# Kernel optimization log

Measured on AMD Instinct MI355X. Metric: run time of the kernel, lower is better.

## Reference

```python
import jax, jax.numpy as jnp
import numpy as np

B, S, D = 4, 512, 256
H_SP, W_SP = 64, 64
NUM_HEADS = 8
HEAD_DIM = D // NUM_HEADS


def setup_inputs() -> dict:
    key = jax.random.key(0)
    ks = jax.random.split(key, 10)
    scale = 1.0 / np.sqrt(D)
    return {
        "query": jax.random.normal(ks[0], (B, S, D), dtype=jnp.float32),
        "key_value": jax.random.normal(ks[1], (B, D, H_SP, W_SP), dtype=jnp.float32),
        "Wq": jax.random.normal(ks[2], (D, D), dtype=jnp.float32) * scale,
        "bq": jnp.zeros((D,), dtype=jnp.float32),
        "Wk": jax.random.normal(ks[3], (D, D), dtype=jnp.float32) * scale,
        "bk": jnp.zeros((D,), dtype=jnp.float32),
        "Wv": jax.random.normal(ks[4], (D, D), dtype=jnp.float32) * scale,
        "bv": jnp.zeros((D,), dtype=jnp.float32),
        "Wo": jax.random.normal(ks[5], (D, D), dtype=jnp.float32) * scale,
        "bo": jnp.zeros((D,), dtype=jnp.float32),
    }


def reference(query, key_value, Wq, bq, Wk, bk, Wv, bv, Wo, bo):
    # query: (B, S, D); key_value: (B, D, H, W)
    b, d, h, w = key_value.shape
    s = query.shape[1]
    hw = h * w
    kv = key_value.reshape(b, d, hw).transpose(0, 2, 1)  # (B, HW, D)

    # Linear projections (torch Linear: x @ W.T + b)
    Q = query @ Wq.T + bq                                # (B, S, D)
    K = kv @ Wk.T + bk                                   # (B, HW, D)
    V = kv @ Wv.T + bv                                   # (B, HW, D)

    # Split heads: (B, nH, len, hd)
    Qh = Q.reshape(b, s, NUM_HEADS, HEAD_DIM).transpose(0, 2, 1, 3)
    Kh = K.reshape(b, hw, NUM_HEADS, HEAD_DIM).transpose(0, 2, 1, 3)
    Vh = V.reshape(b, hw, NUM_HEADS, HEAD_DIM).transpose(0, 2, 1, 3)

    scale = HEAD_DIM ** -0.5
    # NOTE: _add_spatial_attention is dead code (returns attn unchanged);
    # norm1/norm2 are never applied in forward; dropout is identity in eval.
    attn = jnp.einsum('bhsd,bhkd->bhsk', Qh, Kh) * scale  # (B, nH, S, HW)
    attn = jax.nn.softmax(attn, axis=-1)
    out = jnp.einsum('bhsk,bhkd->bhsd', attn, Vh)         # (B, nH, S, hd)
    out = out.transpose(0, 2, 1, 3).reshape(b, s, d)      # (B, S, D)
    return out @ Wo.T + bo
```

## Files before the change

### kernel.cpp

```cpp
#include <hip/hip_runtime.h>

constexpr int B_  = 4;
constexpr int S_  = 512;
constexpr int D_  = 256;
constexpr int HW_ = 4096;
constexpr int NH_ = 8;
constexpr int HD_ = 32;
constexpr int NSPLIT = 2;
constexpr int ROWS_  = B_ * NH_ * S_;
constexpr int KVB    = 64;
constexpr int TILES  = HW_ / NSPLIT / KVB;

typedef float  f32x4  __attribute__((ext_vector_type(4)));
typedef short  s16x4  __attribute__((ext_vector_type(4)));
typedef short  s16x8  __attribute__((ext_vector_type(8)));
typedef __bf16 bf16x8 __attribute__((ext_vector_type(8)));

__device__ __forceinline__ f32x4 mfma_bf16(s16x8 a, s16x8 b, f32x4 c) {
  return __builtin_amdgcn_mfma_f32_16x16x32_bf16(
      __builtin_bit_cast(bf16x8, a), __builtin_bit_cast(bf16x8, b), c, 0, 0, 0);
}

__device__ __forceinline__ void split4(float4 v, s16x4& h, s16x4& l) {
  float x[4] = {v.x, v.y, v.z, v.w};
  #pragma unroll
  for (int j = 0; j < 4; ++j) {
    unsigned xb = __float_as_uint(x[j]);
    h[j] = (short)(xb >> 16);
    float lo = x[j] - __uint_as_float(xb & 0xFFFF0000u);
    l[j] = (short)((__float_as_uint(lo) + 0x8000u) >> 16);
  }
}

__global__ __launch_bounds__(256)
void transpose_split(const float* __restrict__ KV,
                     short* __restrict__ Th, short* __restrict__ Tl)
{
  __shared__ float tile[64][65];
  const int bid = blockIdx.x;
  const int hwb = bid & 63;
  const int db  = (bid >> 6) & 3;
  const int b   = bid >> 8;
  const int hw0 = hwb * 64, d0 = db * 64;
  const int tid = threadIdx.x;
  #pragma unroll
  for (int i = 0; i < 4; ++i) {
    const int idx = tid + (i << 8);
    const int d = idx >> 4, h4 = idx & 15;
    *(float4*)&tile[d][h4 * 4] =
        *(const float4*)&KV[((size_t)(b * D_ + d0 + d)) * HW_ + hw0 + h4 * 4];
  }
  __syncthreads();
  #pragma unroll
  for (int i = 0; i < 4; ++i) {
    const int idx = tid + (i << 8);
    const int hw = idx >> 4, d4 = idx & 15;
    const float4 v = make_float4(tile[d4*4+0][hw], tile[d4*4+1][hw],
                                 tile[d4*4+2][hw], tile[d4*4+3][hw]);
    s16x4 hh, ll; split4(v, hh, ll);
    const size_t o = ((size_t)(b * HW_ + hw0 + hw)) * D_ + d0 + d4 * 4;
    *(s16x4*)&Th[o] = hh; *(s16x4*)&Tl[o] = ll;
  }
}

template<bool ASPLIT, bool DUAL, bool OSPLIT>
__global__ __launch_bounds__(256)
void gemm_mfma(const float* __restrict__ Af,
               const short* __restrict__ Ah_, const short* __restrict__ Al_,
               const float* __restrict__ W0, const float* __restrict__ b0,
               float* __restrict__ C0f, short* __restrict__ C0h, short* __restrict__ C0l,
               const float* __restrict__ W1, const float* __restrict__ b1,
               short* __restrict__ C1h, short* __restrict__ C1l,
               int M, float alpha)
{
  union Sm {
    struct {
      short Ah[64][40], Al[64][40];
      short W0h[64][40], W0l[64][40];
      short W1h[64][40], W1l[64][40];
    } s;
    float ep[64][76];
  };
  __shared__ __align__(16) Sm sm;

  const int tid = threadIdx.x;
  const int wv = tid >> 6, lane = tid & 63, lq = lane & 15, lg = lane >> 4;
  const int wm = wv >> 1, wn = wv & 1;
  const int nx = M >> 6;
  int bid = blockIdx.x;
  bid = (bid & 7) * ((nx << 2) >> 3) + (bid >> 3);
  const int xm = bid % nx, yn = bid / nx;
  const int m0 = xm << 6, n0 = yn << 6;

  f32x4 acc0[2][2] = {};
  f32x4 acc1[2][2] = {};

  s16x8 aH, aL;
  float4 aF[2], w0R[2], w1R[2];

  auto gload = [&](int kt) {
    const int k0 = kt << 5;
    if constexpr (ASPLIT) {
      const int m = tid >> 2, c8 = tid & 3;
      const size_t off = (size_t)(m0 + m) * D_ + k0 + c8 * 8;
      aH = *(const s16x8*)&Ah_[off];
      aL = *(const s16x8*)&Al_[off];
    } else {
      #pragma unroll
      for (int i = 0; i < 2; ++i) {
        const int idx = tid + (i << 8);
        const int m = idx >> 3, c4 = idx & 7;
        aF[i] = *(const float4*)&Af[(size_t)(m0 + m) * D_ + k0 + c4 * 4];
      }
    }
    #pragma unroll
    for (int i = 0; i < 2; ++i) {
      const int idx = tid + (i << 8);
      const int n = idx >> 3, c4 = idx & 7;
      w0R[i] = *(const float4*)&W0[(size_t)(n0 + n) * D_ + k0 + c4 * 4];
      if constexpr (DUAL)
        w1R[i] = *(const float4*)&W1[(size_t)(n0 + n) * D_ + k0 + c4 * 4];
    }
  };

  auto stage = [&]() {
    if constexpr (ASPLIT) {
      const int m = tid >> 2, c8 = tid & 3;
      *(s16x8*)&sm.s.Ah[m][c8 * 8] = aH;
      *(s16x8*)&sm.s.Al[m][c8 * 8] = aL;
    } else {
      #pragma unroll
      for (int i = 0; i < 2; ++i) {
        const int idx = tid + (i << 8);
        const int m = idx >> 3, c4 = idx & 7;
        s16x4 hh, ll; split4(aF[i], hh, ll);
        *(s16x4*)&sm.s.Ah[m][c4 * 4] = hh;
        *(s16x4*)&sm.s.Al[m][c4 * 4] = ll;
      }
    }
    #pragma unroll
    for (int i = 0; i < 2; ++i) {
      const int idx = tid + (i << 8);
      const int n = idx >> 3, c4 = idx & 7;
      float4 w = w0R[i];
      w.x *= alpha; w.y *= alpha; w.z *= alpha; w.w *= alpha;
      s16x4 hh, ll; split4(w, hh, ll);
      *(s16x4*)&sm.s.W0h[n][c4 * 4] = hh;
      *(s16x4*)&sm.s.W0l[n][c4 * 4] = ll;
      if constexpr (DUAL) {
        split4(w1R[i], hh, ll);
        *(s16x4*)&sm.s.W1h[n][c4 * 4] = hh;
        *(s16x4*)&sm.s.W1l[n][c4 * 4] = ll;
      }
    }
  };

  gload(0);
  #pragma unroll
  for (int kt = 0; kt < 8; ++kt) {
    __syncthreads();
    stage();
    __syncthreads();
    if (kt < 7) gload(kt + 1);
    s16x8 ah[2], al[2];
    #pragma unroll
    for (int mi = 0; mi < 2; ++mi) {
      ah[mi] = *(const s16x8*)&sm.s.Ah[wm * 32 + mi * 16 + lq][lg * 8];
      al[mi] = *(const s16x8*)&sm.s.Al[wm * 32 + mi * 16 + lq][lg * 8];
    }
    #pragma unroll
    for (int ni = 0; ni < 2; ++ni) {
      const int nr = wn * 32 + ni * 16 + lq;
      const s16x8 bh = *(const s16x8*)&sm.s.W0h[nr][lg * 8];
      const s16x8 bl = *(const s16x8*)&sm.s.W0l[nr][lg * 8];
      #pragma unroll
      for (int mi = 0; mi < 2; ++mi) {
        acc0[mi][ni] = mfma_bf16(ah[mi], bh, acc0[mi][ni]);
        acc0[mi][ni] = mfma_bf16(al[mi], bh, acc0[mi][ni]);
        acc0[mi][ni] = mfma_bf16(ah[mi], bl, acc0[mi][ni]);
      }
      if constexpr (DUAL) {
        const s16x8 ch = *(const s16x8*)&sm.s.W1h[nr][lg * 8];
        const s16x8 cl = *(const s16x8*)&sm.s.W1l[nr][lg * 8];
        #pragma unroll
        for (int mi = 0; mi < 2; ++mi) {
          acc1[mi][ni] = mfma_bf16(ah[mi], ch, acc1[mi][ni]);
          acc1[mi][ni] = mfma_bf16(al[mi], ch, acc1[mi][ni]);
          acc1[mi][ni] = mfma_bf16(ah[mi], cl, acc1[mi][ni]);
        }
      }
    }
  }

  __syncthreads();
  #pragma unroll
  for (int mi = 0; mi < 2; ++mi)
    #pragma unroll
    for (int ni = 0; ni < 2; ++ni)
      #pragma unroll
      for (int r = 0; r < 4; ++r)
        sm.ep[wm*32 + mi*16 + lg*4 + r][wn*32 + ni*16 + lq] = acc0[mi][ni][r];
  __syncthreads();
  #pragma unroll
  for (int i = 0; i < 4; ++i) {
    const int idx = tid + (i << 8);
    const int m = idx >> 4, c4 = idx & 15;
    const float4 v = *(const float4*)&sm.ep[m][c4 * 4];
    const float4 bb = *(const float4*)&b0[n0 + c4 * 4];
    const float4 o = make_float4(v.x + alpha * bb.x, v.y + alpha * bb.y,
                                 v.z + alpha * bb.z, v.w + alpha * bb.w);
    const size_t off = (size_t)(m0 + m) * D_ + n0 + c4 * 4;
    if constexpr (OSPLIT) {
      s16x4 hh, ll; split4(o, hh, ll);
      *(s16x4*)&C0h[off] = hh;
      *(s16x4*)&C0l[off] = ll;
    } else {
      *(float4*)&C0f[off] = o;
    }
  }

  if constexpr (DUAL) {
    __syncthreads();
    #pragma unroll
    for (int mi = 0; mi < 2; ++mi)
      #pragma unroll
      for (int ni = 0; ni < 2; ++ni)
        *(f32x4*)&sm.ep[wn*32 + ni*16 + lq][wm*32 + mi*16 + lg*4] = acc1[mi][ni];
    __syncthreads();
    const int b = m0 >> 12, hw0 = m0 & (HW_ - 1);
    #pragma unroll
    for (int i = 0; i < 4; ++i) {
      const int idx = tid + (i << 8);
      const int n = idx >> 4, m4 = idx & 15;
      const float4 v = *(const float4*)&sm.ep[n][m4 * 4];
      const float bb = b1[n0 + n];
      const float4 o = make_float4(v.x + bb, v.y + bb, v.z + bb, v.w + bb);
      s16x4 hh, ll; split4(o, hh, ll);
      const size_t off = ((size_t)(b * D_ + n0 + n)) * HW_ + hw0 + m4 * 4;
      *(s16x4*)&C1h[off] = hh;
      *(s16x4*)&C1l[off] = ll;
    }
  }
}

__global__ __launch_bounds__(256)
void attn_mfma(const short* __restrict__ Qh_, const short* __restrict__ Ql_,
               const short* __restrict__ Kh_, const short* __restrict__ Kl_,
               const short* __restrict__ Vth, const short* __restrict__ Vtl,
               float* __restrict__ Opart, float* __restrict__ Ml)
{
  union SmemT {
    struct {
      short Kh[KVB][40], Kl[KVB][40];
      short Vh[HD_][72], Vl[HD_][72];
      short Ph[4][16][72], Pl[4][16][72];
    } a;
    float ep[4][16][36];
  };
  __shared__ __align__(16) SmemT sm;

  const int tid  = threadIdx.x;
  const int wv   = tid >> 6, lane = tid & 63;
  const int lq   = lane & 15, lg = lane >> 4;

  int bid = blockIdx.x;
  bid = (bid & 7) * 64 + (bid >> 3);
  const int qt = bid & 7;
  const int h  = (bid >> 3) & 7;
  const int b  = (bid >> 6) & 3;
  const int sp = bid >> 8;
  const int q0 = qt * 64;

  s16x8 qh, ql;
  {
    const size_t qb = ((size_t)(b * S_ + q0 + wv * 16 + lq)) * D_ + h * HD_ + lg * 8;
    qh = *(const s16x8*)&Qh_[qb];
    ql = *(const s16x8*)&Ql_[qb];
  }

  float mrun = -1e30f, lrun = 0.f;
  f32x4 o0 = {0.f, 0.f, 0.f, 0.f}, o1 = {0.f, 0.f, 0.f, 0.f};

  s16x8 krH, krL, vrH, vrL;
  const int key = tid >> 2, c8k = tid & 3;
  const int dd  = tid >> 3, c8v = tid & 7;
  auto gload = [&](int t) {
    const size_t kb = ((size_t)(b * HW_ + t * KVB + key)) * D_ + h * HD_ + c8k * 8;
    krH = *(const s16x8*)&Kh_[kb];
    krL = *(const s16x8*)&Kl_[kb];
    const size_t vb = ((size_t)(b * D_ + h * HD_ + dd)) * HW_ + t * KVB + c8v * 8;
    vrH = *(const s16x8*)&Vth[vb];
    vrL = *(const s16x8*)&Vtl[vb];
  };

  gload(sp * TILES);
  for (int tt = 0; tt < TILES; ++tt) {
    __syncthreads();
    *(s16x8*)&sm.a.Kh[key][c8k * 8] = krH;
    *(s16x8*)&sm.a.Kl[key][c8k * 8] = krL;
    *(s16x8*)&sm.a.Vh[dd][c8v * 8]  = vrH;
    *(s16x8*)&sm.a.Vl[dd][c8v * 8]  = vrL;
    __syncthreads();
    if (tt + 1 < TILES) gload(sp * TILES + tt + 1);

    f32x4 sc4[4];
    #pragma unroll
    for (int c = 0; c < 4; ++c) {
      const s16x8 ah = *(const s16x8*)&sm.a.Kh[c * 16 + lq][lg * 8];
      const s16x8 al = *(const s16x8*)&sm.a.Kl[c * 16 + lq][lg * 8];
      f32x4 acc = {0.f, 0.f, 0.f, 0.f};
      acc = mfma_bf16(ah, qh, acc);
      acc = mfma_bf16(al, qh, acc);
      acc = mfma_bf16(ah, ql, acc);
      sc4[c] = acc;
    }

    float mt = sc4[0][0];
    #pragma unroll
    for (int c = 0; c < 4; ++c)
      #pragma unroll
      for (int r = 0; r < 4; ++r) mt = fmaxf(mt, sc4[c][r]);
    mt = fmaxf(mt, __shfl_xor(mt, 16));
    mt = fmaxf(mt, __shfl_xor(mt, 32));
    const float nm = fmaxf(mrun, mt);
    const float fr = __expf(mrun - nm);
    mrun = nm;
    o0 *= fr; o1 *= fr;
    float ps = 0.f;
    #pragma unroll
    for (int c = 0; c < 4; ++c) {
      float4 p;
      p.x = __expf(sc4[c][0] - nm);
      p.y = __expf(sc4[c][1] - nm);
      p.z = __expf(sc4[c][2] - nm);
      p.w = __expf(sc4[c][3] - nm);
      ps += p.x + p.y + p.z + p.w;
      s16x4 ph, pl;
      split4(p, ph, pl);
      *(s16x4*)&sm.a.Ph[wv][lq][c * 16 + lg * 4] = ph;
      *(s16x4*)&sm.a.Pl[wv][lq][c * 16 + lg * 4] = pl;
    }
    ps += __shfl_xor(ps, 16);
    ps += __shfl_xor(ps, 32);
    lrun = lrun * fr + ps;

    #pragma unroll
    for (int c2 = 0; c2 < 2; ++c2) {
      const s16x8 ph = *(const s16x8*)&sm.a.Ph[wv][lq][c2 * 32 + lg * 8];
      const s16x8 pl = *(const s16x8*)&sm.a.Pl[wv][lq][c2 * 32 + lg * 8];
      {
        const s16x8 vh = *(const s16x8*)&sm.a.Vh[lq][c2 * 32 + lg * 8];
        const s16x8 vl = *(const s16x8*)&sm.a.Vl[lq][c2 * 32 + lg * 8];
        o0 = mfma_bf16(vh, ph, o0);
        o0 = mfma_bf16(vl, ph, o0);
        o0 = mfma_bf16(vh, pl, o0);
      }
      {
        const s16x8 vh = *(const s16x8*)&sm.a.Vh[16 + lq][c2 * 32 + lg * 8];
        const s16x8 vl = *(const s16x8*)&sm.a.Vl[16 + lq][c2 * 32 + lg * 8];
        o1 = mfma_bf16(vh, ph, o1);
        o1 = mfma_bf16(vl, ph, o1);
        o1 = mfma_bf16(vh, pl, o1);
      }
    }
  }

  __syncthreads();
  #pragma unroll
  for (int r = 0; r < 4; ++r) {
    sm.ep[wv][lq][lg * 4 + r]      = o0[r];
    sm.ep[wv][lq][16 + lg * 4 + r] = o1[r];
  }
  if (lane < 16) {
    const int g = (b * NH_ + h) * S_ + q0 + wv * 16 + lq;
    Ml[((size_t)sp * ROWS_ + g) * 2 + 0] = mrun;
    Ml[((size_t)sp * ROWS_ + g) * 2 + 1] = lrun;
  }
  const int qq = lane >> 2, dq = (lane & 3) * 8;
  const int g2 = (b * NH_ + h) * S_ + q0 + wv * 16 + qq;
  const float4 a0 = *(const float4*)&sm.ep[wv][qq][dq];
  const float4 a1 = *(const float4*)&sm.ep[wv][qq][dq + 4];
  float* dst = &Opart[((size_t)sp * ROWS_ + g2) * HD_ + dq];
  *(float4*)dst       = a0;
  *(float4*)(dst + 4) = a1;
}

__global__ __launch_bounds__(256)
void attn_combine(const float* __restrict__ Opart, const float* __restrict__ Ml,
                  short* __restrict__ AOh, short* __restrict__ AOl)
{
  const int idx = blockIdx.x * 256 + threadIdx.x;
  const int g  = idx >> 3;
  const int c4 = idx & 7;

  float M = -1e30f;
  #pragma unroll
  for (int s = 0; s < NSPLIT; ++s)
    M = fmaxf(M, Ml[((size_t)s * ROWS_ + g) * 2]);

  float4 acc = make_float4(0.f, 0.f, 0.f, 0.f);
  float L = 0.f;
  #pragma unroll
  for (int s = 0; s < NSPLIT; ++s) {
    const size_t base = (size_t)s * ROWS_ + g;
    const float w = __expf(Ml[base * 2] - M);
    L += Ml[base * 2 + 1] * w;
    const float4 o = *(const float4*)&Opart[base * HD_ + c4 * 4];
    acc.x += o.x * w; acc.y += o.y * w; acc.z += o.z * w; acc.w += o.w * w;
  }
  const float inv = 1.0f / L;

  const int q  = g & (S_ - 1);
  const int bh = g >> 9;
  const int h  = bh & (NH_ - 1);
  const int b  = bh >> 3;
  const float4 r = make_float4(acc.x * inv, acc.y * inv, acc.z * inv, acc.w * inv);
  s16x4 hh, ll; split4(r, hh, ll);
  const size_t o = (size_t)(b * S_ + q) * D_ + h * HD_ + c4 * 4;
  *(s16x4*)&AOh[o] = hh;
  *(s16x4*)&AOl[o] = ll;
}

extern "C" void kernel_launch(void* const* d_in, const int* in_sizes, int n_in,
                              void* d_out, int out_size, void* d_ws, size_t ws_size,
                              hipStream_t stream)
{
  const float* query = (const float*)d_in[0];
  const float* keyva = (const float*)d_in[1];
  const float* Wq = (const float*)d_in[2];
  const float* bq = (const float*)d_in[3];
  const float* Wk = (const float*)d_in[4];
  const float* bk = (const float*)d_in[5];
  const float* Wv = (const float*)d_in[6];
  const float* bv = (const float*)d_in[7];
  const float* Wo = (const float*)d_in[8];
  const float* bo = (const float*)d_in[9];
  float* out = (float*)d_out;

  char* w = (char*)d_ws;
  short* KvtH = (short*)w; w += 8388608;
  short* KvtL = (short*)w; w += 8388608;
  short* Qh   = (short*)w; w += 1048576;
  short* Ql   = (short*)w; w += 1048576;
  short* Kh   = (short*)w; w += 8388608;
  short* Kl   = (short*)w; w += 8388608;
  short* VtH  = (short*)w; w += 8388608;
  short* VtL  = (short*)w; w += 8388608;
  short* AOh  = (short*)w; w += 1048576;
  short* AOl  = (short*)w; w += 1048576;
  float* Opart= (float*)KvtH;
  float* Ml   = (float*)((char*)KvtH + 4194304);

  const dim3 blk(256);
  const float qscale = 0.17677669529663687f;

  transpose_split<<<dim3(1024), blk, 0, stream>>>(keyva, KvtH, KvtL);

  gemm_mfma<true, true, true><<<dim3(1024), blk, 0, stream>>>(
      nullptr, KvtH, KvtL, Wk, bk, nullptr, Kh, Kl, Wv, bv, VtH, VtL,
      B_ * HW_, 1.0f);

  gemm_mfma<false, false, true><<<dim3(128), blk, 0, stream>>>(
      query, nullptr, nullptr, Wq, bq, nullptr, Qh, Ql, nullptr, nullptr,
      nullptr, nullptr, B_ * S_, qscale);

  attn_mfma<<<dim3(NSPLIT * B_ * NH_ * (S_ / 64)), blk, 0, stream>>>(
      Qh, Ql, Kh, Kl, VtH, VtL, Opart, Ml);

  attn_combine<<<dim3(ROWS_ * HD_ / 4 / 256), blk, 0, stream>>>(Opart, Ml, AOh, AOl);

  gemm_mfma<true, false, false><<<dim3(128), blk, 0, stream>>>(
      nullptr, AOh, AOl, Wo, bo, out, nullptr, nullptr, nullptr, nullptr,
      nullptr, nullptr, B_ * S_, 1.0f);
}
```

Measured before the change: 184.4 us.

## Rewrite attention with 32x32 MFMA, register-resident P, direct K loads, double-buffered V

Replaces the 16x16x32 MFMA attention kernel with one using 32x32x16 bf16 MFMA, where each wave handles 32 query rows. Probabilities stay in registers and are repacked into B-operand layout with permlane32_swap instead of a round trip through LDS. K is read straight from global memory into MFMA operands rather than staged in shared memory, and V is double-buffered in LDS so only one barrier per tile is needed. NSPLIT goes from 2 to 4 so the grid stays large despite 128 query rows per block, which adds combine traffic and workspace use. The Ml buffer moves to KvtL to fit the larger partial outputs.

```diff
diff --git a/kernel.cpp b/kernel.cpp
--- a/kernel.cpp
+++ b/kernel.cpp
@@ -6,18 +6,25 @@
 constexpr int HW_ = 4096;
 constexpr int NH_ = 8;
 constexpr int HD_ = 32;
-constexpr int NSPLIT = 2;
+constexpr int NSPLIT = 4;
 constexpr int ROWS_  = B_ * NH_ * S_;
 constexpr int KVB    = 64;
 constexpr int TILES  = HW_ / NSPLIT / KVB;
 
-typedef float  f32x4  __attribute__((ext_vector_type(4)));
-typedef short  s16x4  __attribute__((ext_vector_type(4)));
-typedef short  s16x8  __attribute__((ext_vector_type(8)));
-typedef __bf16 bf16x8 __attribute__((ext_vector_type(8)));
+typedef float  f32x4   __attribute__((ext_vector_type(4)));
+typedef float  f32x16  __attribute__((ext_vector_type(16)));
+typedef short  s16x4   __attribute__((ext_vector_type(4)));
+typedef short  s16x8   __attribute__((ext_vector_type(8)));
+typedef __bf16 bf16x8  __attribute__((ext_vector_type(8)));
+typedef unsigned int u32x2 __attribute__((ext_vector_type(2)));
+typedef unsigned int u32x4 __attribute__((ext_vector_type(4)));
 
 __device__ __forceinline__ f32x4 mfma_bf16(s16x8 a, s16x8 b, f32x4 c) {
   return __builtin_amdgcn_mfma_f32_16x16x32_bf16(
+      __builtin_bit_cast(bf16x8, a), __builtin_bit_cast(bf16x8, b), c, 0, 0, 0);
+}
+__device__ __forceinline__ f32x16 mfma32(s16x8 a, s16x8 b, f32x16 c) {
+  return __builtin_amdgcn_mfma_f32_32x32x16_bf16(
       __builtin_bit_cast(bf16x8, a), __builtin_bit_cast(bf16x8, b), c, 0, 0, 0);
 }
 
@@ -30,6 +37,15 @@
     float lo = x[j] - __uint_as_float(xb & 0xFFFF0000u);
     l[j] = (short)((__float_as_uint(lo) + 0x8000u) >> 16);
   }
+}
+
+__device__ __forceinline__ unsigned pk_hi(float x, float y) {
+  return (__float_as_uint(x) >> 16) | (__float_as_uint(y) & 0xFFFF0000u);
+}
+__device__ __forceinline__ unsigned pk_lo(float x, float y) {
+  float rx = x - __uint_as_float(__float_as_uint(x) & 0xFFFF0000u);
+  float ry = y - __uint_as_float(__float_as_uint(y) & 0xFFFF0000u);
+  return (__float_as_uint(rx) >> 16) | (__float_as_uint(ry) & 0xFFFF0000u);
 }
 
 __global__ __launch_bounds__(256)
@@ -244,145 +260,147 @@
 }
 
 __global__ __launch_bounds__(256)
-void attn_mfma(const short* __restrict__ Qh_, const short* __restrict__ Ql_,
-               const short* __restrict__ Kh_, const short* __restrict__ Kl_,
-               const short* __restrict__ Vth, const short* __restrict__ Vtl,
-               float* __restrict__ Opart, float* __restrict__ Ml)
+void attn_mfma32(const short* __restrict__ Qh_, const short* __restrict__ Ql_,
+                 const short* __restrict__ Kh_, const short* __restrict__ Kl_,
+                 const short* __restrict__ Vth, const short* __restrict__ Vtl,
+                 float* __restrict__ Opart, float* __restrict__ Ml)
 {
-  union SmemT {
-    struct {
-      short Kh[KVB][40], Kl[KVB][40];
-      short Vh[HD_][72], Vl[HD_][72];
-      short Ph[4][16][72], Pl[4][16][72];
-    } a;
-    float ep[4][16][36];
-  };
-  __shared__ __align__(16) SmemT sm;
+  union Sm {
+    short V[2][2][32][72];
+    float ep[4][32][33];
+  };
+  __shared__ __align__(16) Sm sm;
 
   const int tid  = threadIdx.x;
   const int wv   = tid >> 6, lane = tid & 63;
-  const int lq   = lane & 15, lg = lane >> 4;
-
-  int bid = blockIdx.x;
-  bid = (bid & 7) * 64 + (bid >> 3);
-  const int qt = bid & 7;
-  const int h  = (bid >> 3) & 7;
-  const int b  = (bid >> 6) & 3;
-  const int sp = bid >> 8;
-  const int q0 = qt * 64;
-
-  s16x8 qh, ql;
+  const int lq   = lane & 31, hi = lane >> 5;
+
+  int w = blockIdx.x;
+  w = (w & 7) * 64 + (w >> 3);
+  const int qt = w & 3;
+  const int h  = (w >> 2) & 7;
+  const int b  = (w >> 5) & 3;
+  const int sp = w >> 7;
+  const int q0 = qt * 128 + wv * 32;
+
+  s16x8 qh[2], ql[2];
   {
-    const size_t qb = ((size_t)(b * S_ + q0 + wv * 16 + lq)) * D_ + h * HD_ + lg * 8;
-    qh = *(const s16x8*)&Qh_[qb];
-    ql = *(const s16x8*)&Ql_[qb];
-  }
-
+    const size_t qb = ((size_t)(b * S_ + q0 + lq)) * D_ + h * HD_ + hi * 8;
+    qh[0] = *(const s16x8*)&Qh_[qb];      qh[1] = *(const s16x8*)&Qh_[qb + 16];
+    ql[0] = *(const s16x8*)&Ql_[qb];      ql[1] = *(const s16x8*)&Ql_[qb + 16];
+  }
+
+  f32x16 o = {0.f,0.f,0.f,0.f, 0.f,0.f,0.f,0.f, 0.f,0.f,0.f,0.f, 0.f,0.f,0.f,0.f};
   float mrun = -1e30f, lrun = 0.f;
-  f32x4 o0 = {0.f, 0.f, 0.f, 0.f}, o1 = {0.f, 0.f, 0.f, 0.f};
-
-  s16x8 krH, krL, vrH, vrL;
-  const int key = tid >> 2, c8k = tid & 3;
-  const int dd  = tid >> 3, c8v = tid & 7;
-  auto gload = [&](int t) {
-    const size_t kb = ((size_t)(b * HW_ + t * KVB + key)) * D_ + h * HD_ + c8k * 8;
-    krH = *(const s16x8*)&Kh_[kb];
-    krL = *(const s16x8*)&Kl_[kb];
-    const size_t vb = ((size_t)(b * D_ + h * HD_ + dd)) * HW_ + t * KVB + c8v * 8;
-    vrH = *(const s16x8*)&Vth[vb];
-    vrL = *(const s16x8*)&Vtl[vb];
-  };
-
-  gload(sp * TILES);
+
+  const int dd = tid >> 3, c8 = tid & 7;
+  s16x8 vrH, vrL;
+  auto gloadV = [&](int t) {
+    const size_t a = ((size_t)(b * D_ + h * HD_ + dd)) * HW_ + (size_t)t * KVB + c8 * 8;
+    vrH = *(const s16x8*)&Vth[a];
+    vrL = *(const s16x8*)&Vtl[a];
+  };
+  auto writeV = [&](int p) {
+    *(s16x8*)&sm.V[p][0][dd][c8 * 8] = vrH;
+    *(s16x8*)&sm.V[p][1][dd][c8 * 8] = vrL;
+  };
+
+  int p = 0;
+  gloadV(sp * TILES);
+  writeV(0);
+
   for (int tt = 0; tt < TILES; ++tt) {
+    const int t = sp * TILES + tt;
+    if (tt + 1 < TILES) gloadV(t + 1);
     __syncthreads();
-    *(s16x8*)&sm.a.Kh[key][c8k * 8] = krH;
-    *(s16x8*)&sm.a.Kl[key][c8k * 8] = krL;
-    *(s16x8*)&sm.a.Vh[dd][c8v * 8]  = vrH;
-    *(s16x8*)&sm.a.Vl[dd][c8v * 8]  = vrL;
-    __syncthreads();
-    if (tt + 1 < TILES) gload(sp * TILES + tt + 1);
-
-    f32x4 sc4[4];
-    #pragma unroll
-    for (int c = 0; c < 4; ++c) {
-      const s16x8 ah = *(const s16x8*)&sm.a.Kh[c * 16 + lq][lg * 8];
-      const s16x8 al = *(const s16x8*)&sm.a.Kl[c * 16 + lq][lg * 8];
-      f32x4 acc = {0.f, 0.f, 0.f, 0.f};
-      acc = mfma_bf16(ah, qh, acc);
-      acc = mfma_bf16(al, qh, acc);
-      acc = mfma_bf16(ah, ql, acc);
-      sc4[c] = acc;
-    }
-
-    float mt = sc4[0][0];
-    #pragma unroll
-    for (int c = 0; c < 4; ++c)
-      #pragma unroll
-      for (int r = 0; r < 4; ++r) mt = fmaxf(mt, sc4[c][r]);
-    mt = fmaxf(mt, __shfl_xor(mt, 16));
+
+    f32x16 sc[2];
+    #pragma unroll
+    for (int cc = 0; cc < 2; ++cc) {
+      const size_t kb = ((size_t)(b * HW_ + t * KVB + cc * 32 + lq)) * D_ + h * HD_ + hi * 8;
+      const s16x8 kh0 = *(const s16x8*)&Kh_[kb];
+      const s16x8 kh1 = *(const s16x8*)&Kh_[kb + 16];
+      const s16x8 kl0 = *(const s16x8*)&Kl_[kb];
+      const s16x8 kl1 = *(const s16x8*)&Kl_[kb + 16];
+      f32x16 a = {0.f,0.f,0.f,0.f, 0.f,0.f,0.f,0.f, 0.f,0.f,0.f,0.f, 0.f,0.f,0.f,0.f};
+      a = mfma32(kh0, qh[0], a);
+      a = mfma32(kh1, qh[1], a);
+      a = mfma32(kl0, qh[0], a);
+      a = mfma32(kl1, qh[1], a);
+      a = mfma32(kh0, ql[0], a);
+      a = mfma32(kh1, ql[1], a);
+      sc[cc] = a;
+    }
+
+    float mt = sc[0][0];
+    #pragma unroll
+    for (int cc = 0; cc < 2; ++cc)
+      #pragma unroll
+      for (int r = 0; r < 16; ++r) mt = fmaxf(mt, sc[cc][r]);
     mt = fmaxf(mt, __shfl_xor(mt, 32));
     const float nm = fmaxf(mrun, mt);
     const float fr = __expf(mrun - nm);
     mrun = nm;
-    o0 *= fr; o1 *= fr;
+    o *= fr;
     float ps = 0.f;
     #pragma unroll
-    for (int c = 0; c < 4; ++c) {
-      float4 p;
-      p.x = __expf(sc4[c][0] - nm);
-      p.y = __expf(sc4[c][1] - nm);
-      p.z = __expf(sc4[c][2] - nm);
-      p.w = __expf(sc4[c][3] - nm);
-      ps += p.x + p.y + p.z + p.w;
-      s16x4 ph, pl;
-      split4(p, ph, pl);
-      *(s16x4*)&sm.a.Ph[wv][lq][c * 16 + lg * 4] = ph;
-      *(s16x4*)&sm.a.Pl[wv][lq][c * 16 + lg * 4] = pl;
-    }
-    ps += __shfl_xor(ps, 16);
+    for (int cc = 0; cc < 2; ++cc)
+      #pragma unroll
+      for (int r = 0; r < 16; ++r) {
+        const float e = __expf(sc[cc][r] - nm);
+        sc[cc][r] = e;
+        ps += e;
+      }
     ps += __shfl_xor(ps, 32);
     lrun = lrun * fr + ps;
 
     #pragma unroll
-    for (int c2 = 0; c2 < 2; ++c2) {
-      const s16x8 ph = *(const s16x8*)&sm.a.Ph[wv][lq][c2 * 32 + lg * 8];
-      const s16x8 pl = *(const s16x8*)&sm.a.Pl[wv][lq][c2 * 32 + lg * 8];
-      {
-        const s16x8 vh = *(const s16x8*)&sm.a.Vh[lq][c2 * 32 + lg * 8];
-        const s16x8 vl = *(const s16x8*)&sm.a.Vl[lq][c2 * 32 + lg * 8];
-        o0 = mfma_bf16(vh, ph, o0);
-        o0 = mfma_bf16(vl, ph, o0);
-        o0 = mfma_bf16(vh, pl, o0);
-      }
-      {
-        const s16x8 vh = *(const s16x8*)&sm.a.Vh[16 + lq][c2 * 32 + lg * 8];
-        const s16x8 vl = *(const s16x8*)&sm.a.Vl[16 + lq][c2 * 32 + lg * 8];
-        o1 = mfma_bf16(vh, ph, o1);
-        o1 = mfma_bf16(vl, ph, o1);
-        o1 = mfma_bf16(vh, pl, o1);
-      }
-    }
+    for (int wn = 0; wn < 4; ++wn) {
+      const int cc = wn >> 1, base = (wn & 1) * 8;
+      const unsigned a_h = pk_hi(sc[cc][base+0], sc[cc][base+1]);
+      const unsigned b_h = pk_hi(sc[cc][base+4], sc[cc][base+5]);
+      const unsigned c_h = pk_hi(sc[cc][base+2], sc[cc][base+3]);
+      const unsigned d_h = pk_hi(sc[cc][base+6], sc[cc][base+7]);
+      const unsigned a_l = pk_lo(sc[cc][base+0], sc[cc][base+1]);
+      const unsigned b_l = pk_lo(sc[cc][base+4], sc[cc][base+5]);
+      const unsigned c_l = pk_lo(sc[cc][base+2], sc[cc][base+3]);
+      const unsigned d_l = pk_lo(sc[cc][base+6], sc[cc][base+7]);
+      const u32x2 s1 = __builtin_amdgcn_permlane32_swap(a_h, b_h, false, false);
+      const u32x2 s2 = __builtin_amdgcn_permlane32_swap(c_h, d_h, false, false);
+      const u32x2 s3 = __builtin_amdgcn_permlane32_swap(a_l, b_l, false, false);
+      const u32x2 s4 = __builtin_amdgcn_permlane32_swap(c_l, d_l, false, false);
+      const u32x4 wH = {s1[0], s2[0], s1[1], s2[1]};
+      const u32x4 wL = {s3[0], s4[0], s3[1], s4[1]};
+      const s16x8 pH = __builtin_bit_cast(s16x8, wH);
+      const s16x8 pL = __builtin_bit_cast(s16x8, wL);
+      const s16x8 vh = *(const s16x8*)&sm.V[p][0][lq][wn * 16 + hi * 8];
+      const s16x8 vl = *(const s16x8*)&sm.V[p][1][lq][wn * 16 + hi * 8];
+      o = mfma32(vh, pH, o);
+      o = mfma32(vl, pH, o);
+      o = mfma32(vh, pL, o);
+    }
+
+    if (tt + 1 < TILES) writeV(p ^ 1);
+    p ^= 1;
   }
 
   __syncthreads();
-  #pragma unroll
-  for (int r = 0; r < 4; ++r) {
-    sm.ep[wv][lq][lg * 4 + r]      = o0[r];
-    sm.ep[wv][lq][16 + lg * 4 + r] = o1[r];
-  }
-  if (lane < 16) {
-    const int g = (b * NH_ + h) * S_ + q0 + wv * 16 + lq;
+  if (lane < 32) {
+    const int g = (b * NH_ + h) * S_ + q0 + lq;
     Ml[((size_t)sp * ROWS_ + g) * 2 + 0] = mrun;
     Ml[((size_t)sp * ROWS_ + g) * 2 + 1] = lrun;
   }
-  const int qq = lane >> 2, dq = (lane & 3) * 8;
-  const int g2 = (b * NH_ + h) * S_ + q0 + wv * 16 + qq;
-  const float4 a0 = *(const float4*)&sm.ep[wv][qq][dq];
-  const float4 a1 = *(const float4*)&sm.ep[wv][qq][dq + 4];
-  float* dst = &Opart[((size_t)sp * ROWS_ + g2) * HD_ + dq];
-  *(float4*)dst       = a0;
-  *(float4*)(dst + 4) = a1;
+  #pragma unroll
+  for (int r = 0; r < 16; ++r) {
+    const int d = (r & 3) + 8 * (r >> 2) + 4 * hi;
+    sm.ep[wv][lq][d] = o[r];
+  }
+  const int qq = lane >> 1, d0 = (lane & 1) * 16;
+  const int g2 = (b * NH_ + h) * S_ + q0 + qq;
+  float* dst = &Opart[((size_t)sp * ROWS_ + g2) * HD_ + d0];
+  #pragma unroll
+  for (int j = 0; j < 4; ++j)
+    *(float4*)(dst + j * 4) = *(const float4*)&sm.ep[wv][qq][d0 + j * 4];
 }
 
 __global__ __launch_bounds__(256)
@@ -449,7 +467,7 @@
   short* AOh  = (short*)w; w += 1048576;
   short* AOl  = (short*)w; w += 1048576;
   float* Opart= (float*)KvtH;
-  float* Ml   = (float*)((char*)KvtH + 4194304);
+  float* Ml   = (float*)KvtL;
 
   const dim3 blk(256);
   const float qscale = 0.17677669529663687f;
@@ -464,7 +482,7 @@
       query, nullptr, nullptr, Wq, bq, nullptr, Qh, Ql, nullptr, nullptr,
       nullptr, nullptr, B_ * S_, qscale);
 
-  attn_mfma<<<dim3(NSPLIT * B_ * NH_ * (S_ / 64)), blk, 0, stream>>>(
+  attn_mfma32<<<dim3(NSPLIT * B_ * NH_ * (S_ / 128)), blk, 0, stream>>>(
       Qh, Ql, Kh, Kl, VtH, VtL, Opart, Ml);
 
   attn_combine<<<dim3(ROWS_ * HD_ / 4 / 256), blk, 0, stream>>>(Opart, Ml, AOh, AOl);
```

New measurement: 177.2 us. 1.04x faster.
